# Performance work log

Measured on AMD Instinct MI355X. Metric: run time of the kernel, lower is better.

The kernel has to match this reference:

```python
import jax, jax.numpy as jnp
import numpy as np

B, T, I, H, L, O = 512, 512, 64, 256, 3, 1  # batch, seq_len, input, hidden, layers, output


def setup_inputs() -> dict:
    key = jax.random.key(0)
    ks = jax.random.split(key, 16)
    s = 1.0 / np.sqrt(H)  # PyTorch nn.RNN init: U(-1/sqrt(H), 1/sqrt(H))
    u = lambda k, shape: jax.random.uniform(k, shape, jnp.float32, -s, s)
    inp = {"x": jax.random.normal(ks[0], (B, T, I), jnp.float32)}
    in_sizes = [I, H, H]
    for l in range(L):
        inp[f"w_ih{l}"] = u(ks[1 + 4 * l], (H, in_sizes[l]))
        inp[f"w_hh{l}"] = u(ks[2 + 4 * l], (H, H))
        inp[f"b_ih{l}"] = u(ks[3 + 4 * l], (H,))
        inp[f"b_hh{l}"] = u(ks[4 + 4 * l], (H,))
    inp["w_fc"] = u(ks[13], (O, H))
    inp["b_fc"] = u(ks[14], (O,))
    return inp


def _rnn_layer(x, w_ih, w_hh, b_ih, b_hh):
    # x: [B, T, in] -> outputs [B, T, H]; h_t = tanh(x_t W_ih^T + b_ih + h_{t-1} W_hh^T + b_hh)
    pre = jnp.einsum('bti,hi->bth', x, w_ih) + b_ih + b_hh  # input projection for all t at once

    def step(h, p_t):
        h = jnp.tanh(p_t + h @ w_hh.T)
        return h, h

    h0 = jnp.zeros((x.shape[0], w_hh.shape[0]), x.dtype)
    _, ys = jax.lax.scan(step, h0, pre.transpose(1, 0, 2))  # scan over time
    return ys.transpose(1, 0, 2)


def reference(x, w_ih0, w_hh0, b_ih0, b_hh0, w_ih1, w_hh1, b_ih1, b_hh1,
              w_ih2, w_hh2, b_ih2, b_hh2, w_fc, b_fc):
    h = _rnn_layer(x, w_ih0, w_hh0, b_ih0, b_hh0)
    h = _rnn_layer(h, w_ih1, w_hh1, b_ih1, b_hh1)
    h = _rnn_layer(h, w_ih2, w_hh2, b_ih2, b_hh2)
    out = h[:, -1, :] @ w_fc.T + b_fc  # [B, 1]
    return out.squeeze()  # [B]
```

## Files before the change

kernel.cpp:

```cpp
#include <hip/hip_runtime.h>
#include <cstdint>
#include <cstddef>

#define Tsz 512
#define TC  32
#define NCH 16

typedef _Float16 f16;
typedef _Float16 half8_t __attribute__((ext_vector_type(8)));
typedef _Float16 half4_t __attribute__((ext_vector_type(4)));
typedef float float4_t __attribute__((ext_vector_type(4)));

__device__ __forceinline__ float fast_exp2(float x) {
  float r;
  asm("v_exp_f32 %0, %1" : "=v"(r) : "v"(x));
  return r;
}
__device__ __forceinline__ void pin(half8_t& v) { asm("" : "+v"(v)); }

#define BARRIER_LG asm volatile("s_waitcnt lgkmcnt(0)\n\ts_barrier" ::: "memory")

template<int LAYER>
__device__ __forceinline__ void layer_body(
    char* const smem, const int chunk, const int tile,
    const float* __restrict__ x,
    const f16* inbuf,
    const f16* __restrict__ wih_h, const f16* __restrict__ whh_h,
    const float* __restrict__ biasc,
    f16* outbuf,
    f16* st)
{
  constexpr int NIN = (LAYER == 0) ? 2 : 8;
  char* const h_lds = smem;

  const int tid  = threadIdx.x;
  const int lane = tid & 63;
  const int wave = tid >> 6;
  const int m    = lane & 15;
  const int q    = lane >> 4;
  const int lo   = m * 16;
  const int t0   = chunk * TC;
  const int slot = chunk & 1;

  half8_t whh[2][8], wih[2][NIN];
  float bias[2];
#pragma unroll
  for (int jt = 0; jt < 2; ++jt) {
    const int j = wave * 32 + jt * 16 + m;
    bias[jt] = biasc[LAYER * 256 + j];
#pragma unroll
    for (int c = 0; c < 8; ++c)
      whh[jt][c] = *(const half8_t*)(whh_h + j * 256 + c * 32 + q * 8);
#pragma unroll
    for (int c = 0; c < NIN; ++c)
      wih[jt][c] = *(const half8_t*)(wih_h + j * (NIN * 32) + c * 32 + q * 8);
  }
#pragma unroll
  for (int jt = 0; jt < 2; ++jt) {
#pragma unroll
    for (int c = 0; c < 8; ++c) pin(whh[jt][c]);
#pragma unroll
    for (int c = 0; c < NIN; ++c) pin(wih[jt][c]);
  }

  if (chunk == 0)
    *(float4_t*)(h_lds + tid * 16) = float4_t{0.f, 0.f, 0.f, 0.f};
  else
    *(float4_t*)(h_lds + tid * 16) = *(const float4_t*)((const char*)st + tile * 8192 + tid * 16);

  float4_t  xp[2][4];
  half8_t   xq[2][8];
  auto xload = [&](int t, float4_t* d) {
    const int tc = (t > Tsz - 1) ? (Tsz - 1) : t;
    const float* base = x + ((size_t)(tile * 16 + m) * Tsz + tc) * 64 + q * 8;
    d[0] = *(const float4_t*)base;        d[1] = *(const float4_t*)(base + 4);
    d[2] = *(const float4_t*)(base + 32); d[3] = *(const float4_t*)(base + 36);
  };
  auto xqload = [&](int tl, half8_t* d) {
    const int tn = (tl > TC - 1) ? (TC - 1) : tl;
    const char* gb = (const char*)inbuf + (((size_t)(tile * 2 + slot) * TC + tn) << 13) + lo;
#pragma unroll
    for (int c = 0; c < 8; ++c)
      d[c] = *(const half8_t*)(gb + (c * 4 + q) * 256);
  };

  if constexpr (LAYER == 0) { xload(t0, xp[0]); xload(t0 + 1, xp[1]); }
  else                      { xqload(0, xq[0]); xqload(1, xq[1]); }
  BARRIER_LG;

#pragma unroll 4
  for (int tl = 0; tl < TC; ++tl) {
    char* cur = h_lds + (tl & 1) * 8192;
    char* nxt = h_lds + ((tl + 1) & 1) * 8192;

    half8_t xf[NIN];
    if constexpr (LAYER == 0) {
      const float4_t* xr = xp[tl & 1];
#pragma unroll
      for (int c = 0; c < 2; ++c)
#pragma unroll
        for (int u = 0; u < 8; ++u) xf[c][u] = (f16)xr[c * 2 + (u >> 2)][u & 3];
      xload(t0 + tl + 2, xp[tl & 1]);
    } else {
#pragma unroll
      for (int c = 0; c < 8; ++c) xf[c] = xq[tl & 1][c];
      xqload(tl + 2, xq[tl & 1]);
    }
    half8_t hf[8];
#pragma unroll
    for (int c = 0; c < 8; ++c) hf[c] = *(const half8_t*)(cur + (c * 4 + q) * 256 + lo);

    float4_t acc[2];
#pragma unroll
    for (int jt = 0; jt < 2; ++jt) {
      float4_t a0 = {bias[jt], bias[jt], bias[jt], bias[jt]};
      float4_t a1 = {0.f, 0.f, 0.f, 0.f};
#pragma unroll
      for (int c = 0; c < NIN; ++c)
        a0 = __builtin_amdgcn_mfma_f32_16x16x32_f16(xf[c], wih[jt][c], a0, 0, 0, 0);
#pragma unroll
      for (int c = 0; c < 8; ++c)
        a1 = __builtin_amdgcn_mfma_f32_16x16x32_f16(hf[c], whh[jt][c], a1, 0, 0, 0);
      acc[jt] = a0 + a1;
    }

#pragma unroll
    for (int jt = 0; jt < 2; ++jt) {
      const int j = wave * 32 + jt * 16 + m;
#pragma unroll
      for (int r = 0; r < 4; ++r) {
        const float e    = fast_exp2(acc[jt][r] * 2.8853900817779268f);
        const float hval = 1.0f - 2.0f * __builtin_amdgcn_rcpf(1.0f + e);
        const int b = q * 4 + r;
        *(f16*)(nxt + (j >> 3) * 256 + b * 16 + (j & 7) * 2) = (f16)hval;
      }
    }

    BARRIER_LG;

    if constexpr (LAYER < 2) {
      char* gp = (char*)outbuf + (((size_t)(tile * 2 + slot) * TC + tl) << 13) + tid * 16;
      *(float4_t*)gp = *(const float4_t*)(nxt + tid * 16);
    }
  }

  *(float4_t*)((char*)st + tile * 8192 + tid * 16) = *(const float4_t*)(h_lds + tid * 16);
}

__global__ __launch_bounds__(512, 1)
void rnn_chunk_kernel(const float* __restrict__ x,
                      f16* bufA, f16* bufB,
                      const f16* __restrict__ wih0h, const f16* __restrict__ whh0h,
                      const f16* __restrict__ wih1h, const f16* __restrict__ whh1h,
                      const f16* __restrict__ wih2h, const f16* __restrict__ whh2h,
                      const float* __restrict__ biasc,
                      f16* st0, f16* st1, f16* st2, int k)
{
  __shared__ __align__(16) char smem[16384];
  const int layer = blockIdx.x >> 5;
  const int tile  = blockIdx.x & 31;
  const int chunk = k - layer;
  if (chunk < 0 || chunk >= NCH) return;
  if (layer == 0)
    layer_body<0>(smem, chunk, tile, x, nullptr, wih0h, whh0h, biasc, bufA, st0);
  else if (layer == 1)
    layer_body<1>(smem, chunk, tile, nullptr, bufA, wih1h, whh1h, biasc, bufB, st1);
  else
    layer_body<2>(smem, chunk, tile, nullptr, bufB, wih2h, whh2h, biasc, nullptr, st2);
}

__global__ void prep_kernel(const float* __restrict__ wih0, const float* __restrict__ whh0,
                            const float* __restrict__ bih0, const float* __restrict__ bhh0,
                            const float* __restrict__ wih1, const float* __restrict__ whh1,
                            const float* __restrict__ bih1, const float* __restrict__ bhh1,
                            const float* __restrict__ wih2, const float* __restrict__ whh2,
                            const float* __restrict__ bih2, const float* __restrict__ bhh2,
                            f16* wih0h, f16* whh0h, f16* wih1h, f16* whh1h,
                            f16* wih2h, f16* whh2h, float* biasc)
{
  const int i = blockIdx.x * 256 + threadIdx.x;
  if      (i < 16384)  wih0h[i]          = (f16)wih0[i];
  else if (i < 81920)  whh0h[i - 16384]  = (f16)whh0[i - 16384];
  else if (i < 147456) wih1h[i - 81920]  = (f16)wih1[i - 81920];
  else if (i < 212992) whh1h[i - 147456] = (f16)whh1[i - 147456];
  else if (i < 278528) wih2h[i - 212992] = (f16)wih2[i - 212992];
  else if (i < 344064) whh2h[i - 278528] = (f16)whh2[i - 278528];
  else if (i < 344320) biasc[i - 344064]       = bih0[i - 344064] + bhh0[i - 344064];
  else if (i < 344576) biasc[256 + i - 344320] = bih1[i - 344320] + bhh1[i - 344320];
  else if (i < 344832) biasc[512 + i - 344576] = bih2[i - 344576] + bhh2[i - 344576];
}

__global__ void fc_kernel(const f16* __restrict__ st2, const float* __restrict__ w_fc,
                          const float* __restrict__ b_fc, float* __restrict__ outp) {
  const int b = blockIdx.x;
  const int lane = threadIdx.x;
  const int tile = b >> 4, bl = b & 15;
  const int j = lane * 4;
  const char* hp = (const char*)st2 + tile * 8192 + (j >> 3) * 256 + bl * 16 + (j & 7) * 2;
  const half4_t hv = *(const half4_t*)hp;
  const float4_t w = *(const float4_t*)(w_fc + j);
  float s = (float)hv[0] * w[0] + (float)hv[1] * w[1] + (float)hv[2] * w[2] + (float)hv[3] * w[3];
#pragma unroll
  for (int off = 32; off > 0; off >>= 1) s += __shfl_down(s, off, 64);
  if (lane == 0) outp[b] = s + b_fc[0];
}

extern "C" void kernel_launch(void* const* d_in, const int* in_sizes, int n_in,
                              void* d_out, int out_size, void* d_ws, size_t ws_size,
                              hipStream_t stream) {
  const float* x     = (const float*)d_in[0];
  const float* w_ih0 = (const float*)d_in[1];
  const float* w_hh0 = (const float*)d_in[2];
  const float* b_ih0 = (const float*)d_in[3];
  const float* b_hh0 = (const float*)d_in[4];
  const float* w_ih1 = (const float*)d_in[5];
  const float* w_hh1 = (const float*)d_in[6];
  const float* b_ih1 = (const float*)d_in[7];
  const float* b_hh1 = (const float*)d_in[8];
  const float* w_ih2 = (const float*)d_in[9];
  const float* w_hh2 = (const float*)d_in[10];
  const float* b_ih2 = (const float*)d_in[11];
  const float* b_hh2 = (const float*)d_in[12];
  const float* w_fc  = (const float*)d_in[13];
  const float* b_fc  = (const float*)d_in[14];

  char* ws = (char*)d_ws;
  f16* bufA   = (f16*)(ws);
  f16* bufB   = (f16*)(ws + 16777216);
  f16* st0    = (f16*)(ws + 33554432);
  f16* st1    = (f16*)(ws + 33816576);
  f16* st2    = (f16*)(ws + 34078720);
  f16* wih0h  = (f16*)(ws + 34340864);
  f16* whh0h  = (f16*)(ws + 34373632);
  f16* wih1h  = (f16*)(ws + 34504704);
  f16* whh1h  = (f16*)(ws + 34635776);
  f16* wih2h  = (f16*)(ws + 34766848);
  f16* whh2h  = (f16*)(ws + 34897920);
  float* biasc = (float*)(ws + 35028992);

  prep_kernel<<<1347, 256, 0, stream>>>(w_ih0, w_hh0, b_ih0, b_hh0,
                                        w_ih1, w_hh1, b_ih1, b_hh1,
                                        w_ih2, w_hh2, b_ih2, b_hh2,
                                        wih0h, whh0h, wih1h, whh1h, wih2h, whh2h, biasc);
  for (int k = 0; k < NCH + 2; ++k)
    rnn_chunk_kernel<<<96, 512, 0, stream>>>(x, bufA, bufB,
                                             wih0h, whh0h, wih1h, whh1h, wih2h, whh2h,
                                             biasc, st0, st1, st2, k);
  fc_kernel<<<512, 64, 0, stream>>>(st2, w_fc, b_fc, (float*)d_out);
}
```

Measured before the change: 1.079 ms.

## Move input projections off the recurrent critical path into producer layers

Each layer's recurrence now consumes a precomputed fp32 pre-activation buffer (input projection plus bias) instead of doing the input-projection MFMAs itself. Layers 0 and 1 compute the next layer's projection from their fresh hidden state, one step behind, off the serial dependency. Layer 2 blocks compute layer 0's projection from x for a future chunk, and a new pre0 kernel seeds the first chunk. This shortens the per-step serial MFMA chain at the cost of fp32 intermediate buffers with twice the memory traffic and an extra launch.

```diff
diff --git a/kernel.cpp b/kernel.cpp
--- a/kernel.cpp
+++ b/kernel.cpp
@@ -12,55 +12,47 @@
 typedef float float4_t __attribute__((ext_vector_type(4)));
 
 __device__ __forceinline__ float fast_exp2(float x) {
-  float r;
-  asm("v_exp_f32 %0, %1" : "=v"(r) : "v"(x));
-  return r;
+  float r; asm("v_exp_f32 %0, %1" : "=v"(r) : "v"(x)); return r;
 }
 __device__ __forceinline__ void pin(half8_t& v) { asm("" : "+v"(v)); }
 
 #define BARRIER_LG asm volatile("s_waitcnt lgkmcnt(0)\n\ts_barrier" ::: "memory")
 
+__device__ __forceinline__ size_t poff(int tile, int slot, int t, int j, int q) {
+  return (((size_t)((tile * 2 + slot) * TC + t) * 256 + j) << 6) + ((size_t)q << 4);
+}
+
 template<int LAYER>
-__device__ __forceinline__ void layer_body(
+__device__ __forceinline__ void rec01_body(
     char* const smem, const int chunk, const int tile,
-    const float* __restrict__ x,
-    const f16* inbuf,
-    const f16* __restrict__ wih_h, const f16* __restrict__ whh_h,
-    const float* __restrict__ biasc,
-    f16* outbuf,
-    f16* st)
-{
-  constexpr int NIN = (LAYER == 0) ? 2 : 8;
+    const float* __restrict__ Pin, float* __restrict__ Pout,
+    const f16* __restrict__ whh_h, const f16* __restrict__ wihn_h,
+    const float* __restrict__ biasc, f16* __restrict__ st)
+{
   char* const h_lds = smem;
-
   const int tid  = threadIdx.x;
   const int lane = tid & 63;
   const int wave = tid >> 6;
   const int m    = lane & 15;
   const int q    = lane >> 4;
   const int lo   = m * 16;
-  const int t0   = chunk * TC;
   const int slot = chunk & 1;
 
-  half8_t whh[2][8], wih[2][NIN];
-  float bias[2];
+  half8_t whh[2][8], wihn[2][8];
+  float biasn[2];
 #pragma unroll
   for (int jt = 0; jt < 2; ++jt) {
     const int j = wave * 32 + jt * 16 + m;
-    bias[jt] = biasc[LAYER * 256 + j];
-#pragma unroll
-    for (int c = 0; c < 8; ++c)
-      whh[jt][c] = *(const half8_t*)(whh_h + j * 256 + c * 32 + q * 8);
-#pragma unroll
-    for (int c = 0; c < NIN; ++c)
-      wih[jt][c] = *(const half8_t*)(wih_h + j * (NIN * 32) + c * 32 + q * 8);
+    biasn[jt] = biasc[(LAYER + 1) * 256 + j];
+#pragma unroll
+    for (int c = 0; c < 8; ++c) whh[jt][c]  = *(const half8_t*)(whh_h  + j * 256 + c * 32 + q * 8);
+#pragma unroll
+    for (int c = 0; c < 8; ++c) wihn[jt][c] = *(const half8_t*)(wihn_h + j * 256 + c * 32 + q * 8);
   }
 #pragma unroll
   for (int jt = 0; jt < 2; ++jt) {
 #pragma unroll
-    for (int c = 0; c < 8; ++c) pin(whh[jt][c]);
-#pragma unroll
-    for (int c = 0; c < NIN; ++c) pin(wih[jt][c]);
+    for (int c = 0; c < 8; ++c) { pin(whh[jt][c]); pin(wihn[jt][c]); }
   }
 
   if (chunk == 0)
@@ -68,24 +60,14 @@
   else
     *(float4_t*)(h_lds + tid * 16) = *(const float4_t*)((const char*)st + tile * 8192 + tid * 16);
 
-  float4_t  xp[2][4];
-  half8_t   xq[2][8];
-  auto xload = [&](int t, float4_t* d) {
-    const int tc = (t > Tsz - 1) ? (Tsz - 1) : t;
-    const float* base = x + ((size_t)(tile * 16 + m) * Tsz + tc) * 64 + q * 8;
-    d[0] = *(const float4_t*)base;        d[1] = *(const float4_t*)(base + 4);
-    d[2] = *(const float4_t*)(base + 32); d[3] = *(const float4_t*)(base + 36);
+  float4_t pld[2][2];
+  auto pload = [&](int tl, float4_t* d) {
+    const int tn = (tl > TC - 1) ? (TC - 1) : tl;
+    const char* gb = (const char*)Pin + poff(tile, slot, tn, wave * 32 + m, q);
+    d[0] = *(const float4_t*)gb;
+    d[1] = *(const float4_t*)(gb + 1024);
   };
-  auto xqload = [&](int tl, half8_t* d) {
-    const int tn = (tl > TC - 1) ? (TC - 1) : tl;
-    const char* gb = (const char*)inbuf + (((size_t)(tile * 2 + slot) * TC + tn) << 13) + lo;
-#pragma unroll
-    for (int c = 0; c < 8; ++c)
-      d[c] = *(const half8_t*)(gb + (c * 4 + q) * 256);
-  };
-
-  if constexpr (LAYER == 0) { xload(t0, xp[0]); xload(t0 + 1, xp[1]); }
-  else                      { xqload(0, xq[0]); xqload(1, xq[1]); }
+  pload(0, pld[0]); pload(1, pld[1]);
   BARRIER_LG;
 
 #pragma unroll 4
@@ -93,19 +75,6 @@
     char* cur = h_lds + (tl & 1) * 8192;
     char* nxt = h_lds + ((tl + 1) & 1) * 8192;
 
-    half8_t xf[NIN];
-    if constexpr (LAYER == 0) {
-      const float4_t* xr = xp[tl & 1];
-#pragma unroll
-      for (int c = 0; c < 2; ++c)
-#pragma unroll
-        for (int u = 0; u < 8; ++u) xf[c][u] = (f16)xr[c * 2 + (u >> 2)][u & 3];
-      xload(t0 + tl + 2, xp[tl & 1]);
-    } else {
-#pragma unroll
-      for (int c = 0; c < 8; ++c) xf[c] = xq[tl & 1][c];
-      xqload(tl + 2, xq[tl & 1]);
-    }
     half8_t hf[8];
 #pragma unroll
     for (int c = 0; c < 8; ++c) hf[c] = *(const half8_t*)(cur + (c * 4 + q) * 256 + lo);
@@ -113,15 +82,23 @@
     float4_t acc[2];
 #pragma unroll
     for (int jt = 0; jt < 2; ++jt) {
-      float4_t a0 = {bias[jt], bias[jt], bias[jt], bias[jt]};
-      float4_t a1 = {0.f, 0.f, 0.f, 0.f};
-#pragma unroll
-      for (int c = 0; c < NIN; ++c)
-        a0 = __builtin_amdgcn_mfma_f32_16x16x32_f16(xf[c], wih[jt][c], a0, 0, 0, 0);
+      float4_t a = pld[tl & 1][jt];
 #pragma unroll
       for (int c = 0; c < 8; ++c)
-        a1 = __builtin_amdgcn_mfma_f32_16x16x32_f16(hf[c], whh[jt][c], a1, 0, 0, 0);
-      acc[jt] = a0 + a1;
+        a = __builtin_amdgcn_mfma_f32_16x16x32_f16(hf[c], whh[jt][c], a, 0, 0, 0);
+      acc[jt] = a;
+    }
+    pload(tl + 2, pld[tl & 1]);
+
+    if (tl >= 1) {
+#pragma unroll
+      for (int jt = 0; jt < 2; ++jt) {
+        float4_t b = {biasn[jt], biasn[jt], biasn[jt], biasn[jt]};
+#pragma unroll
+        for (int c = 0; c < 8; ++c)
+          b = __builtin_amdgcn_mfma_f32_16x16x32_f16(hf[c], wihn[jt][c], b, 0, 0, 0);
+        *(float4_t*)((char*)Pout + poff(tile, slot, tl - 1, wave * 32 + jt * 16 + m, q)) = b;
+      }
     }
 
 #pragma unroll
@@ -129,44 +106,185 @@
       const int j = wave * 32 + jt * 16 + m;
 #pragma unroll
       for (int r = 0; r < 4; ++r) {
-        const float e    = fast_exp2(acc[jt][r] * 2.8853900817779268f);
-        const float hval = 1.0f - 2.0f * __builtin_amdgcn_rcpf(1.0f + e);
+        const float e  = fast_exp2(acc[jt][r] * 2.8853900817779268f);
+        const float hv = 1.0f - 2.0f * __builtin_amdgcn_rcpf(1.0f + e);
         const int b = q * 4 + r;
-        *(f16*)(nxt + (j >> 3) * 256 + b * 16 + (j & 7) * 2) = (f16)hval;
-      }
-    }
-
+        *(f16*)(nxt + (j >> 3) * 256 + b * 16 + (j & 7) * 2) = (f16)hv;
+      }
+    }
     BARRIER_LG;
-
-    if constexpr (LAYER < 2) {
-      char* gp = (char*)outbuf + (((size_t)(tile * 2 + slot) * TC + tl) << 13) + tid * 16;
-      *(float4_t*)gp = *(const float4_t*)(nxt + tid * 16);
-    }
-  }
-
+  }
+
+  {
+    half8_t hf[8];
+#pragma unroll
+    for (int c = 0; c < 8; ++c) hf[c] = *(const half8_t*)(h_lds + (c * 4 + q) * 256 + lo);
+#pragma unroll
+    for (int jt = 0; jt < 2; ++jt) {
+      float4_t b = {biasn[jt], biasn[jt], biasn[jt], biasn[jt]};
+#pragma unroll
+      for (int c = 0; c < 8; ++c)
+        b = __builtin_amdgcn_mfma_f32_16x16x32_f16(hf[c], wihn[jt][c], b, 0, 0, 0);
+      *(float4_t*)((char*)Pout + poff(tile, slot, TC - 1, wave * 32 + jt * 16 + m, q)) = b;
+    }
+  }
   *(float4_t*)((char*)st + tile * 8192 + tid * 16) = *(const float4_t*)(h_lds + tid * 16);
+}
+
+template<bool REC, bool PRE>
+__device__ __forceinline__ void l2_body(
+    char* const smem, const int chunk, const int pre_chunk, const int tile,
+    const float* __restrict__ x, const float* __restrict__ Pin, float* __restrict__ Pout,
+    const f16* __restrict__ whh_h, const f16* __restrict__ wih0_h,
+    const float* __restrict__ biasc, f16* __restrict__ st)
+{
+  char* const h_lds = smem;
+  const int tid  = threadIdx.x;
+  const int lane = tid & 63;
+  const int wave = tid >> 6;
+  const int m    = lane & 15;
+  const int q    = lane >> 4;
+  const int lo   = m * 16;
+  const int slot  = chunk & 1;
+  const int pslot = pre_chunk & 1;
+
+  half8_t whh[2][8], wih0[2][2];
+  float bias0[2];
+#pragma unroll
+  for (int jt = 0; jt < 2; ++jt) {
+    const int j = wave * 32 + jt * 16 + m;
+    if constexpr (PRE) {
+      bias0[jt] = biasc[j];
+#pragma unroll
+      for (int c = 0; c < 2; ++c) wih0[jt][c] = *(const half8_t*)(wih0_h + j * 64 + c * 32 + q * 8);
+    }
+    if constexpr (REC) {
+#pragma unroll
+      for (int c = 0; c < 8; ++c) whh[jt][c] = *(const half8_t*)(whh_h + j * 256 + c * 32 + q * 8);
+    }
+  }
+#pragma unroll
+  for (int jt = 0; jt < 2; ++jt) {
+    if constexpr (REC) {
+#pragma unroll
+      for (int c = 0; c < 8; ++c) pin(whh[jt][c]);
+    }
+    if constexpr (PRE) { pin(wih0[jt][0]); pin(wih0[jt][1]); }
+  }
+
+  float4_t pld[2][2];
+  auto pload = [&](int tl, float4_t* d) {
+    const int tn = (tl > TC - 1) ? (TC - 1) : tl;
+    const char* gb = (const char*)Pin + poff(tile, slot, tn, wave * 32 + m, q);
+    d[0] = *(const float4_t*)gb;
+    d[1] = *(const float4_t*)(gb + 1024);
+  };
+  float4_t xp[2][4];
+  auto xload = [&](int tl, float4_t* d) {
+    const int tn = (tl > TC - 1) ? (TC - 1) : tl;
+    const float* base = x + ((size_t)(tile * 16 + m) * Tsz + (pre_chunk * TC + tn)) * 64 + q * 8;
+    d[0] = *(const float4_t*)base;        d[1] = *(const float4_t*)(base + 4);
+    d[2] = *(const float4_t*)(base + 32); d[3] = *(const float4_t*)(base + 36);
+  };
+
+  if constexpr (REC) {
+    if (chunk == 0)
+      *(float4_t*)(h_lds + tid * 16) = float4_t{0.f, 0.f, 0.f, 0.f};
+    else
+      *(float4_t*)(h_lds + tid * 16) = *(const float4_t*)((const char*)st + tile * 8192 + tid * 16);
+    pload(0, pld[0]); pload(1, pld[1]);
+  }
+  if constexpr (PRE) { xload(0, xp[0]); xload(1, xp[1]); }
+  if constexpr (REC) BARRIER_LG;
+
+#pragma unroll 4
+  for (int tl = 0; tl < TC; ++tl) {
+    if constexpr (REC) {
+      char* cur = h_lds + (tl & 1) * 8192;
+      char* nxt = h_lds + ((tl + 1) & 1) * 8192;
+      half8_t hf[8];
+#pragma unroll
+      for (int c = 0; c < 8; ++c) hf[c] = *(const half8_t*)(cur + (c * 4 + q) * 256 + lo);
+      float4_t acc[2];
+#pragma unroll
+      for (int jt = 0; jt < 2; ++jt) {
+        float4_t a = pld[tl & 1][jt];
+#pragma unroll
+        for (int c = 0; c < 8; ++c)
+          a = __builtin_amdgcn_mfma_f32_16x16x32_f16(hf[c], whh[jt][c], a, 0, 0, 0);
+        acc[jt] = a;
+      }
+      pload(tl + 2, pld[tl & 1]);
+#pragma unroll
+      for (int jt = 0; jt < 2; ++jt) {
+        const int j = wave * 32 + jt * 16 + m;
+#pragma unroll
+        for (int r = 0; r < 4; ++r) {
+          const float e  = fast_exp2(acc[jt][r] * 2.8853900817779268f);
+          const float hv = 1.0f - 2.0f * __builtin_amdgcn_rcpf(1.0f + e);
+          const int b = q * 4 + r;
+          *(f16*)(nxt + (j >> 3) * 256 + b * 16 + (j & 7) * 2) = (f16)hv;
+        }
+      }
+    }
+    if constexpr (PRE) {
+      half8_t xf[2];
+      const float4_t* xr = xp[tl & 1];
+#pragma unroll
+      for (int c = 0; c < 2; ++c)
+#pragma unroll
+        for (int u = 0; u < 8; ++u) xf[c][u] = (f16)xr[c * 2 + (u >> 2)][u & 3];
+      xload(tl + 2, xp[tl & 1]);
+#pragma unroll
+      for (int jt = 0; jt < 2; ++jt) {
+        float4_t b = {bias0[jt], bias0[jt], bias0[jt], bias0[jt]};
+#pragma unroll
+        for (int c = 0; c < 2; ++c)
+          b = __builtin_amdgcn_mfma_f32_16x16x32_f16(xf[c], wih0[jt][c], b, 0, 0, 0);
+        *(float4_t*)((char*)Pout + poff(tile, pslot, tl, wave * 32 + jt * 16 + m, q)) = b;
+      }
+    }
+    if constexpr (REC) BARRIER_LG;
+  }
+
+  if constexpr (REC)
+    *(float4_t*)((char*)st + tile * 8192 + tid * 16) = *(const float4_t*)(h_lds + tid * 16);
 }
 
 __global__ __launch_bounds__(512, 1)
 void rnn_chunk_kernel(const float* __restrict__ x,
-                      f16* bufA, f16* bufB,
-                      const f16* __restrict__ wih0h, const f16* __restrict__ whh0h,
-                      const f16* __restrict__ wih1h, const f16* __restrict__ whh1h,
-                      const f16* __restrict__ wih2h, const f16* __restrict__ whh2h,
+                      float* P0, float* P1, float* P2,
+                      const f16* __restrict__ whh0h, const f16* __restrict__ whh1h,
+                      const f16* __restrict__ whh2h, const f16* __restrict__ wih0h,
+                      const f16* __restrict__ wih1h, const f16* __restrict__ wih2h,
                       const float* __restrict__ biasc,
                       f16* st0, f16* st1, f16* st2, int k)
 {
   __shared__ __align__(16) char smem[16384];
   const int layer = blockIdx.x >> 5;
   const int tile  = blockIdx.x & 31;
-  const int chunk = k - layer;
-  if (chunk < 0 || chunk >= NCH) return;
-  if (layer == 0)
-    layer_body<0>(smem, chunk, tile, x, nullptr, wih0h, whh0h, biasc, bufA, st0);
-  else if (layer == 1)
-    layer_body<1>(smem, chunk, tile, nullptr, bufA, wih1h, whh1h, biasc, bufB, st1);
-  else
-    layer_body<2>(smem, chunk, tile, nullptr, bufB, wih2h, whh2h, biasc, nullptr, st2);
+  if (layer == 0) {
+    if (k < NCH) rec01_body<0>(smem, k, tile, P0, P1, whh0h, wih1h, biasc, st0);
+  } else if (layer == 1) {
+    const int c = k - 1;
+    if (c >= 0 && c < NCH) rec01_body<1>(smem, c, tile, P1, P2, whh1h, wih2h, biasc, st1);
+  } else {
+    const int c  = k - 2;
+    const int pc = k + 1;
+    const bool rec = (c >= 0 && c < NCH);
+    const bool pre = (pc < NCH);
+    if (rec && pre)  l2_body<true,  true >(smem, c, pc, tile, x, P2, P0, whh2h, wih0h, biasc, st2);
+    else if (rec)    l2_body<true,  false>(smem, c, pc, tile, x, P2, P0, whh2h, wih0h, biasc, st2);
+    else if (pre)    l2_body<false, true >(smem, c, pc, tile, x, P2, P0, whh2h, wih0h, biasc, st2);
+  }
+}
+
+__global__ __launch_bounds__(512, 1)
+void pre0_kernel(const float* __restrict__ x, float* P0,
+                 const f16* __restrict__ wih0h, const float* __restrict__ biasc)
+{
+  __shared__ __align__(16) char smem[16384];
+  l2_body<false, true>(smem, 0, 0, blockIdx.x, x, nullptr, P0, nullptr, wih0h, biasc, nullptr);
 }
 
 __global__ void prep_kernel(const float* __restrict__ wih0, const float* __restrict__ whh0,
@@ -225,26 +343,29 @@
   const float* b_fc  = (const float*)d_in[14];
 
   char* ws = (char*)d_ws;
-  f16* bufA   = (f16*)(ws);
-  f16* bufB   = (f16*)(ws + 16777216);
-  f16* st0    = (f16*)(ws + 33554432);
-  f16* st1    = (f16*)(ws + 33816576);
-  f16* st2    = (f16*)(ws + 34078720);
-  f16* wih0h  = (f16*)(ws + 34340864);
-  f16* whh0h  = (f16*)(ws + 34373632);
-  f16* wih1h  = (f16*)(ws + 34504704);
-  f16* whh1h  = (f16*)(ws + 34635776);
-  f16* wih2h  = (f16*)(ws + 34766848);
-  f16* whh2h  = (f16*)(ws + 34897920);
-  float* biasc = (float*)(ws + 35028992);
+  float* P0   = (float*)(ws);
+  float* P1   = (float*)(ws + 33554432);
+  float* P2   = (float*)(ws + 67108864);
+  f16* st0    = (f16*)(ws + 100663296);
+  f16* st1    = (f16*)(ws + 100925440);
+  f16* st2    = (f16*)(ws + 101187584);
+  f16* wih0h  = (f16*)(ws + 101449728);
+  f16* whh0h  = (f16*)(ws + 101482496);
+  f16* wih1h  = (f16*)(ws + 101613568);
+  f16* whh1h  = (f16*)(ws + 101744640);
+  f16* wih2h  = (f16*)(ws + 101875712);
+  f16* whh2h  = (f16*)(ws + 102006784);
+  float* biasc = (float*)(ws + 102137856);
 
   prep_kernel<<<1347, 256, 0, stream>>>(w_ih0, w_hh0, b_ih0, b_hh0,
                                         w_ih1, w_hh1, b_ih1, b_hh1,
                                         w_ih2, w_hh2, b_ih2, b_hh2,
                                         wih0h, whh0h, wih1h, whh1h, wih2h, whh2h, biasc);
+  pre0_kernel<<<32, 512, 0, stream>>>(x, P0, wih0h, biasc);
   for (int k = 0; k < NCH + 2; ++k)
-    rnn_chunk_kernel<<<96, 512, 0, stream>>>(x, bufA, bufB,
-                                             wih0h, whh0h, wih1h, whh1h, wih2h, whh2h,
+    rnn_chunk_kernel<<<96, 512, 0, stream>>>(x, P0, P1, P2,
+                                             whh0h, whh1h, whh2h,
+                                             wih0h, wih1h, wih2h,
                                              biasc, st0, st1, st2, k);
   fc_kernel<<<512, 64, 0, stream>>>(st2, w_fc, b_fc, (float*)d_out);
 }
```

Result: faster. 1.032 ms (-4.4%).
